# Kernel optimization log

Measured on AMD Instinct MI355X. Metric: run time of the kernel, lower is better.

Reference implementation:

```python
import jax, jax.numpy as jnp
import numpy as np

B = 8
RESOLUTIONS = [65, 129, 257, 513, 1025]
NUM_POINTS = [0, 4096, 16384, 65536, 262144]
CLIP_MIN = -1e9
FINAL = 1025          # last resolution (both axes)
B_MIN, B_MAX = -1.0, 1.0
BALANCE = 0.5


def setup_inputs() -> dict:
    key = jax.random.key(0)
    k1, k2, k3, k4 = jax.random.split(key, 4)
    return {
        "w1": jax.random.normal(k1, (2, 256), jnp.float32),
        "b1": jax.random.normal(k2, (256,), jnp.float32),
        "w2": jax.random.normal(k3, (256, 1), jnp.float32),
        "b2": jax.random.normal(k4, (1,), jnp.float32),
    }


def _interp_bilinear_ac(x, H, W):
    """F.interpolate(..., mode='bilinear', align_corners=True). x: [B, C, h, w]."""
    b, c, h, w = x.shape
    ys = jnp.linspace(0.0, h - 1.0, H)
    xs = jnp.linspace(0.0, w - 1.0, W)
    y0 = jnp.floor(ys).astype(jnp.int32)
    y1 = jnp.minimum(y0 + 1, h - 1)
    wy = ys - y0
    x0 = jnp.floor(xs).astype(jnp.int32)
    x1 = jnp.minimum(x0 + 1, w - 1)
    wx = xs - x0
    # interpolate rows, then columns
    top = x[:, :, y0, :] * (1.0 - wy)[None, None, :, None] + x[:, :, y1, :] * wy[None, None, :, None]
    return top[:, :, :, x0] * (1.0 - wx) + top[:, :, :, x1] * wx


def _batch_eval(coords, w1, b1, w2, b2):
    """coords: [B, N, 2] in final-resolution pixel space (align_corners=False mapping).
    Returns occupancy [B, N] (C == 1)."""
    coords2d = coords / FINAL + 0.5 / FINAL                 # normalize to [0, 1]
    p = coords2d * (B_MAX - B_MIN) + B_MIN                  # [B, N, 2] in world coords
    h = jax.nn.relu(jnp.einsum('bnd,dh->bnh', p, w1) + b1)  # [B, N, 256]
    occ = jax.nn.sigmoid(jnp.einsum('bnh,ho->bno', h, w2) + b2)
    return occ[..., 0]


def reference(w1, b1, w2, b2):
    occ = None
    for i, res in enumerate(RESOLUTIONS):
        if i == 0:
            # init_coords: grid of res x res points spanning [0, FINAL-1]
            xs = jnp.linspace(0.0, FINAL - 1.0, res)
            gy, gx = jnp.meshgrid(xs, xs, indexing='ij')          # y rows, x cols
            coords = jnp.stack([gx.ravel(), gy.ravel()], axis=-1)  # [N, 2] (x, y)
            coords = jnp.broadcast_to(coords, (B, res * res, 2))
            o = _batch_eval(coords, w1, b1, w2, b2)               # [B, N]
            occ = o.reshape(B, 1, res, res)                       # [B, C, H, W]
        else:
            occ = _interp_bilinear_ac(occ, res, res)
            npt = NUM_POINTS[i]
            if npt <= 0:
                continue
            # uncertainty = -|occ - balance_value|
            unc = -jnp.abs(occ - BALANCE)                          # [B, 1, H, W]
            flat_unc = unc.reshape(B, res * res)
            scores, idx = jax.lax.top_k(flat_unc, npt)             # [B, npt]
            px = (idx % res).astype(jnp.float32)
            py = (idx // res).astype(jnp.float32)
            stride = (FINAL - 1.0) / (res - 1.0)
            coords = jnp.stack([px, py], axis=-1) * stride         # [B, npt, 2]
            new_vals = _batch_eval(coords, w1, b1, w2, b2)         # [B, npt]
            occ_flat = occ.reshape(B, res * res)
            old_vals = jnp.take_along_axis(occ_flat, idx, axis=1)
            vals = jnp.where(scores >= CLIP_MIN, new_vals, old_vals)
            occ_flat = jax.vmap(lambda o, i2, v: o.at[i2].set(v))(occ_flat, idx, vals)
            occ = occ_flat.reshape(B, 1, res, res)
    return occ
```

## Files before the change

kernel.cpp:

```cpp
#include <hip/hip_runtime.h>
#include <stdint.h>

#define HID 256
#define NMAXPIX (1025 * 1025)
#define NREP 8
#define NSEG 2048
#define SELMAX 2112

#define HISTA_OFF 0
#define HISTB_OFF 16384
#define HISTC_OFF 32768
#define SCAL_OFF  40960
#define TIC_OFF   41024
#define STAGE_U32 43072

__device__ __forceinline__ float mlp_eval4(float wx, float wy,
                                           const float4* __restrict__ w1x,
                                           const float4* __restrict__ w1y,
                                           const float4* __restrict__ vb1,
                                           const float4* __restrict__ vw2, float b2v) {
    const float C0 = (float)(0.5 / 1025.0);
    float px = (wx / 1025.0f + C0) * 2.0f - 1.0f;
    float py = (wy / 1025.0f + C0) * 2.0f - 1.0f;
    float a0 = 0.f, a1 = 0.f, a2 = 0.f, a3 = 0.f;
#pragma unroll 8
    for (int q = 0; q < HID / 4; ++q) {
        float4 a = w1x[q], b = w1y[q], c = vb1[q], d = vw2[q];
        float h0 = px * a.x + py * b.x + c.x;
        float h1 = px * a.y + py * b.y + c.y;
        float h2 = px * a.z + py * b.z + c.z;
        float h3 = px * a.w + py * b.w + c.w;
        h0 = h0 > 0.f ? h0 : 0.f;
        h1 = h1 > 0.f ? h1 : 0.f;
        h2 = h2 > 0.f ? h2 : 0.f;
        h3 = h3 > 0.f ? h3 : 0.f;
        a0 += h0 * d.x;
        a1 += h1 * d.y;
        a2 += h2 * d.z;
        a3 += h3 * d.w;
    }
    float x = ((a0 + a1) + (a2 + a3)) + b2v;
    float r;
    if (x >= 0.f) { r = 1.0f / (1.0f + expf(-x)); }
    else { float e = expf(x); r = e / (1.0f + e); }
    return r;
}

__device__ __forceinline__ uint32_t block_exscan_256(uint32_t v, volatile uint32_t* lds4) {
    int lane = threadIdx.x & 63, w = threadIdx.x >> 6;
    uint32_t inc = v;
#pragma unroll
    for (int d = 1; d < 64; d <<= 1) {
        uint32_t o = (uint32_t)__shfl_up((int)inc, d, 64);
        if (lane >= d) inc += o;
    }
    if (lane == 63) lds4[w] = inc;
    __syncthreads();
    uint32_t woff = 0;
    for (int i = 0; i < w; ++i) woff += lds4[i];
    return woff + inc - v;
}

__device__ void scan_dev(const uint32_t* __restrict__ hist, int NB,
                         uint32_t rem_in, uint32_t prefix_in, int shift,
                         uint32_t* outp, uint32_t* outr,
                         volatile uint32_t* lds4, volatile uint32_t* ldspair) {
    int tid = threadIdx.x;
    int C = NB >> 8;
    int b0 = NB - (tid + 1) * C;
    uint32_t cnts[8];
#pragma unroll
    for (int k = 0; k < 8; ++k) cnts[k] = 0;
    for (int rep = 0; rep < NREP; ++rep) {
        const uint4* p = (const uint4*)(hist + (size_t)rep * NB + b0);
#pragma unroll
        for (int g = 0; g < 2; ++g) {
            if (g * 4 < C) {
                uint4 v = p[g];
                cnts[g * 4 + 0] += v.x;
                cnts[g * 4 + 1] += v.y;
                cnts[g * 4 + 2] += v.z;
                cnts[g * 4 + 3] += v.w;
            }
        }
    }
    uint32_t ssum = 0;
    for (int k = 0; k < C; ++k) ssum += cnts[k];
    uint32_t excl = block_exscan_256(ssum, lds4);
    uint32_t run = excl;
    for (int k = 0; k < C; ++k) {
        uint32_t c = cnts[C - 1 - k];
        if (rem_in > run && rem_in <= run + c) {
            ldspair[0] = (prefix_in << shift) | (uint32_t)(b0 + C - 1 - k);
            ldspair[1] = rem_in - run;
        }
        run += c;
    }
    __syncthreads();
    *outp = ldspair[0];
    *outr = ldspair[1];
}

__global__ __launch_bounds__(256) void k_eval0z(const float* __restrict__ w1, const float* __restrict__ b1,
                                                const float* __restrict__ w2, const float* __restrict__ b2,
                                                float* __restrict__ occ, uint32_t* __restrict__ zbuf, int zcount) {
    __shared__ alignas(16) float sw1[2 * HID];
    __shared__ alignas(16) float sb1[HID];
    __shared__ alignas(16) float sw2[HID];
    int tid = threadIdx.x;
    for (int i = tid; i < 2 * HID; i += 256) sw1[i] = w1[i];
    sb1[tid] = b1[tid];
    sw2[tid] = w2[tid];
    __syncthreads();
    int gtid = blockIdx.x * 256 + tid;
    int nthreads = gridDim.x * 256;
    for (int i = gtid; i < zcount; i += nthreads) zbuf[i] = 0;
    for (int n = gtid; n < 65 * 65; n += nthreads) {
        int i = n / 65, j = n % 65;
        occ[n] = mlp_eval4(16.0f * (float)j, 16.0f * (float)i,
                           (const float4*)sw1, (const float4*)(sw1 + HID),
                           (const float4*)sb1, (const float4*)sw2, b2[0]);
    }
}

__global__ __launch_bounds__(256) void k_upkey(const float* __restrict__ in, int rp,
                                               float* __restrict__ outg, int r, int nb, int bstride,
                                               uint32_t* __restrict__ keys,
                                               uint32_t* __restrict__ histA) {
    __shared__ uint32_t hist[2048];
    int tid = threadIdx.x;
    for (int k = tid; k < 2048; k += 256) hist[k] = 0;
    __syncthreads();
    int N = r * r;
    int lane = tid & 63;
    int gstride = gridDim.x * 256;
    for (int n0 = blockIdx.x * 256; n0 < N; n0 += gstride) {
        int n = n0 + tid;
        bool act = n < N;
        uint32_t key = 0;
        if (act) {
            int i = n / r, j = n % r;
            int i2 = i >> 1, j2 = j >> 1;
            float v;
            if ((i & 1) == 0) {
                if ((j & 1) == 0) {
                    v = in[i2 * rp + j2];
                } else {
                    float a = in[i2 * rp + j2], b = in[i2 * rp + j2 + 1];
                    v = a * 0.5f + b * 0.5f;
                }
            } else {
                if ((j & 1) == 0) {
                    float a = in[i2 * rp + j2], b = in[(i2 + 1) * rp + j2];
                    v = a * 0.5f + b * 0.5f;
                } else {
                    float a = in[i2 * rp + j2],      c = in[i2 * rp + j2 + 1];
                    float b = in[(i2 + 1) * rp + j2], d = in[(i2 + 1) * rp + j2 + 1];
                    float t1 = a * 0.5f + b * 0.5f;
                    float t2 = c * 0.5f + d * 0.5f;
                    v = t1 * 0.5f + t2 * 0.5f;
                }
            }
            for (int k = 0; k < nb; ++k) outg[(size_t)k * bstride + n] = v;
            float unc = -fabsf(v - 0.5f);
            uint32_t u = __float_as_uint(unc);
            key = (u & 0x80000000u) ? ~u : (u | 0x80000000u);
            keys[n] = key;
        }
        uint32_t bin = key >> 21;
        unsigned long long m = __ballot(act);
        if (m) {
            int leader = __ffsll(m) - 1;
            uint32_t lbin = (uint32_t)__shfl((int)bin, leader, 64);
            unsigned long long smk = __ballot(act && bin == lbin);
            if (smk == m) {
                if (lane == leader) atomicAdd(&hist[lbin], (uint32_t)__popcll(m));
            } else if (act) {
                atomicAdd(&hist[bin], 1u);
            }
        }
    }
    __syncthreads();
    uint32_t* myrep = histA + (size_t)(blockIdx.x & (NREP - 1)) * 2048;
    for (int k = tid; k < 2048; k += 256) {
        uint32_t c = hist[k];
        if (c) atomicAdd(&myrep[k], c);
    }
}

__global__ __launch_bounds__(256) void k_histmid(const uint32_t* __restrict__ keys, int N,
                                                 const uint32_t* __restrict__ prevHist,
                                                 uint32_t* __restrict__ scal,
                                                 int useNpt, uint32_t npt, int scalInIdx, int shift,
                                                 int scalOutIdx,
                                                 int fshift, int bshift, uint32_t bmask,
                                                 uint32_t* __restrict__ outHist, int NBout) {
    __shared__ uint32_t lh[2048];
    __shared__ uint32_t lds4[4];
    __shared__ uint32_t ldspair[2];
    int tid = threadIdx.x, lane = tid & 63;
    uint32_t rem_in = useNpt ? npt : scal[scalInIdx + 1];
    uint32_t pfx_in = useNpt ? 0u  : scal[scalInIdx];
    uint32_t pfx, rem;
    scan_dev(prevHist, 2048, rem_in, pfx_in, shift, &pfx, &rem, lds4, ldspair);
    if (blockIdx.x == 0 && tid == 0) { scal[scalOutIdx] = pfx; scal[scalOutIdx + 1] = rem; }
    for (int k = tid; k < 2048; k += 256) lh[k] = 0;
    __syncthreads();
    int gstride = gridDim.x * 256;
    for (int base = blockIdx.x * 256; base < N; base += gstride) {
        int n = base + tid;
        bool inb = n < N;
        uint32_t key = inb ? keys[n] : 0u;
        bool flt = inb && ((key >> fshift) == pfx);
        uint32_t bin = (key >> bshift) & bmask;
        unsigned long long m = __ballot(flt);
        if (m) {
            int leader = __ffsll(m) - 1;
            uint32_t lbin = (uint32_t)__shfl((int)bin, leader, 64);
            unsigned long long smk = __ballot(flt && bin == lbin);
            if (smk == m) {
                if (lane == leader) atomicAdd(&lh[lbin], (uint32_t)__popcll(m));
            } else if (flt) {
                atomicAdd(&lh[bin], 1u);
            }
        }
    }
    __syncthreads();
    uint32_t* myrep = outHist + (size_t)(blockIdx.x & (NREP - 1)) * NBout;
    for (int k = tid; k < NBout; k += 256) {
        uint32_t c = lh[k];
        if (c) atomicAdd(&myrep[k], c);
    }
}

__global__ __launch_bounds__(256) void k_segcnt(const uint32_t* __restrict__ keys, int N, int seglen,
                                                const uint32_t* __restrict__ histC,
                                                uint32_t* __restrict__ scal,
                                                uint32_t* __restrict__ tic) {
    __shared__ uint32_t lds4[4];
    __shared__ uint32_t ldspair[2];
    int tid = threadIdx.x, lane = tid & 63;
    uint32_t rem2 = scal[3], pfx2 = scal[2];
    uint32_t K, t;
    scan_dev(histC, 1024, rem2, pfx2, 10, &K, &t, lds4, ldspair);
    if (blockIdx.x == 0 && tid == 0) { scal[4] = K; scal[5] = t; }
    int wv = blockIdx.x * 4 + (tid >> 6);
    int s0 = wv * seglen;
    int s1 = s0 + seglen; if (s1 > N) s1 = N;
    uint32_t tcnt = 0;
    for (int base = s0; base < s1; base += 64) {
        int n = base + lane;
        if (n < s1) tcnt += (keys[n] == K) ? 1u : 0u;
    }
#pragma unroll
    for (int d = 32; d; d >>= 1) tcnt += (uint32_t)__shfl_down((int)tcnt, d, 64);
    if (lane == 0) tic[wv] = tcnt;
}

__global__ __launch_bounds__(256) void k_seleval(const uint32_t* __restrict__ keys, int N, int seglen,
                                                 const uint32_t* __restrict__ scal,
                                                 const uint32_t* __restrict__ tic,
                                                 int r, float stride,
                                                 float* __restrict__ occ, int nb, int bstride,
                                                 const float* __restrict__ w1, const float* __restrict__ b1,
                                                 const float* __restrict__ w2, const float* __restrict__ b2) {
    __shared__ alignas(16) float sw1[2 * HID];
    __shared__ alignas(16) float sb1[HID];
    __shared__ alignas(16) float sw2[HID];
    __shared__ uint32_t selcnt;
    __shared__ uint32_t selidx[SELMAX];
    int tid = threadIdx.x, lane = tid & 63;
    for (int i = tid; i < 2 * HID; i += 256) sw1[i] = w1[i];
    sb1[tid] = b1[tid];
    sw2[tid] = w2[tid];
    if (tid == 0) selcnt = 0;
    __syncthreads();
    uint32_t K = scal[4], t = scal[5];

    int wv = blockIdx.x * 4 + (tid >> 6);
    uint32_t tp = 0;
    for (int i = lane; i < wv; i += 64) tp += tic[i];
#pragma unroll
    for (int d = 32; d; d >>= 1) tp += (uint32_t)__shfl_down((int)tp, d, 64);
    tp = (uint32_t)__shfl((int)tp, 0, 64);

    uint32_t tie_run = tp;
    int s0 = wv * seglen;
    int s1 = s0 + seglen; if (s1 > N) s1 = N;
    unsigned long long lowmask = (lane == 63) ? ~0ull >> 1 : ((1ull << lane) - 1ull);
    for (int base = s0; base < s1; base += 64) {
        int n = base + lane;
        bool inb = n < s1;
        uint32_t key = inb ? keys[n] : 0u;
        bool gt = inb && (key > K);
        bool tie = inb && (key == K);
        unsigned long long tm = __ballot(tie);
        uint32_t trank = tie_run + (uint32_t)__popcll(tm & lowmask);
        bool sel = gt || (tie && trank < t);
        unsigned long long smk = __ballot(sel);
        if (smk) {
            int leader = __ffsll(smk) - 1;
            uint32_t wbase = 0;
            if (lane == leader) wbase = atomicAdd(&selcnt, (uint32_t)__popcll(smk));
            wbase = (uint32_t)__shfl((int)wbase, leader, 64);
            if (sel) selidx[wbase + (uint32_t)__popcll(smk & lowmask)] = (uint32_t)n;
        }
        tie_run += (uint32_t)__popcll(tm);
    }
    __syncthreads();

    uint32_t cnt = selcnt;
    float vb2 = b2[0];
    const float4* w1x = (const float4*)sw1;
    const float4* w1y = (const float4*)(sw1 + HID);
    const float4* vb1 = (const float4*)sb1;
    const float4* vw2 = (const float4*)sw2;
    const float C0 = (float)(0.5 / 1025.0);
    for (uint32_t bb = 0; bb < cnt; bb += 512) {
        uint32_t i0 = bb + tid, i1 = bb + tid + 256;
        bool v0 = i0 < cnt, v1 = i1 < cnt;
        int nA = v0 ? (int)selidx[i0] : 0;
        int nB = v1 ? (int)selidx[i1] : 0;
        int iA = nA / r, jA = nA % r;
        int iB = nB / r, jB = nB % r;
        float pxA = ((stride * (float)jA) / 1025.0f + C0) * 2.0f - 1.0f;
        float pyA = ((stride * (float)iA) / 1025.0f + C0) * 2.0f - 1.0f;
        float pxB = ((stride * (float)jB) / 1025.0f + C0) * 2.0f - 1.0f;
        float pyB = ((stride * (float)iB) / 1025.0f + C0) * 2.0f - 1.0f;
        float4 A0 = {0, 0, 0, 0}, A1 = {0, 0, 0, 0};
#pragma unroll 4
        for (int q = 0; q < HID / 4; ++q) {
            float4 a = w1x[q], b = w1y[q], c = vb1[q], d = vw2[q];
            {
                float h0 = pxA * a.x + pyA * b.x + c.x;
                float h1 = pxA * a.y + pyA * b.y + c.y;
                float h2 = pxA * a.z + pyA * b.z + c.z;
                float h3 = pxA * a.w + pyA * b.w + c.w;
                h0 = h0 > 0.f ? h0 : 0.f;
                h1 = h1 > 0.f ? h1 : 0.f;
                h2 = h2 > 0.f ? h2 : 0.f;
                h3 = h3 > 0.f ? h3 : 0.f;
                A0.x += h0 * d.x; A0.y += h1 * d.y;
                A0.z += h2 * d.z; A0.w += h3 * d.w;
            }
            {
                float h0 = pxB * a.x + pyB * b.x + c.x;
                float h1 = pxB * a.y + pyB * b.y + c.y;
                float h2 = pxB * a.z + pyB * b.z + c.z;
                float h3 = pxB * a.w + pyB * b.w + c.w;
                h0 = h0 > 0.f ? h0 : 0.f;
                h1 = h1 > 0.f ? h1 : 0.f;
                h2 = h2 > 0.f ? h2 : 0.f;
                h3 = h3 > 0.f ? h3 : 0.f;
                A1.x += h0 * d.x; A1.y += h1 * d.y;
                A1.z += h2 * d.z; A1.w += h3 * d.w;
            }
        }
        if (v0) {
            float x = ((A0.x + A0.y) + (A0.z + A0.w)) + vb2;
            float rr;
            if (x >= 0.f) { rr = 1.0f / (1.0f + expf(-x)); }
            else { float e = expf(x); rr = e / (1.0f + e); }
            for (int k = 0; k < nb; ++k) occ[(size_t)k * bstride + nA] = rr;
        }
        if (v1) {
            float x = ((A1.x + A1.y) + (A1.z + A1.w)) + vb2;
            float rr;
            if (x >= 0.f) { rr = 1.0f / (1.0f + expf(-x)); }
            else { float e = expf(x); rr = e / (1.0f + e); }
            for (int k = 0; k < nb; ++k) occ[(size_t)k * bstride + nB] = rr;
        }
    }
}

__global__ __launch_bounds__(256) void k_bcast(const float* __restrict__ src, float* __restrict__ dst, int N) {
    int q = blockIdx.x * 256 + threadIdx.x;
    int n = q * 4;
    if (n + 3 < N) {
        float4 v = *(const float4*)(src + n);
#pragma unroll
        for (int k = 0; k < 8; ++k) *(float4*)(dst + (size_t)k * N + n) = v;
    } else if (n < N) {
        for (int m = n; m < N; ++m) {
            float v = src[m];
#pragma unroll
            for (int k = 0; k < 8; ++k) dst[(size_t)k * N + m] = v;
        }
    }
}

extern "C" void kernel_launch(void* const* d_in, const int* in_sizes, int n_in,
                              void* d_out, int out_size, void* d_ws, size_t ws_size,
                              hipStream_t stream) {
    const float* w1 = (const float*)d_in[0];
    const float* b1 = (const float*)d_in[1];
    const float* w2 = (const float*)d_in[2];
    const float* b2 = (const float*)d_in[3];
    float* out = (float*)d_out;

    const size_t A = (((size_t)NMAXPIX * 4) + 255) & ~(size_t)255;
    const size_t SMALL_BYTES = (size_t)4 * STAGE_U32 * 4;
    const size_t need = 3 * A + SMALL_BYTES;

    int fused8 = (ws_size >= need);
    char* base = fused8 ? (char*)d_ws : (char*)d_out;
    float* buf0 = (float*)(base);
    float* buf1 = (float*)(base + A);
    uint32_t* keys = (uint32_t*)(base + 2 * A);
    uint32_t* smallb = (uint32_t*)(base + 3 * A);

    k_eval0z<<<dim3(512), dim3(256), 0, stream>>>(w1, b1, w2, b2, buf0, smallb, 4 * STAGE_U32);

    const int resA[5] = {65, 129, 257, 513, 1025};
    const int nptA[5] = {0, 4096, 16384, 65536, 262144};
    float* cur = buf0;
    float* nxt = buf1;
    for (int s = 1; s < 5; ++s) {
        int rp = resA[s - 1], r = resA[s];
        int N = r * r;
        uint32_t npt = (uint32_t)nptA[s];
        uint32_t* sm    = smallb + (size_t)(s - 1) * STAGE_U32;
        uint32_t* histA = sm + HISTA_OFF;
        uint32_t* histB = sm + HISTB_OFF;
        uint32_t* histC = sm + HISTC_OFF;
        uint32_t* scal  = sm + SCAL_OFF;
        uint32_t* tic   = sm + TIC_OFF;
        int nb1 = (N + 255) / 256;
        int nbu = nb1 < 1024 ? nb1 : 1024;
        int seglen = (N + NSEG - 1) / NSEG;
        float stride = 1024.0f / (float)(r - 1);

        int last = (s == 4);
        float* stage_out = (last && fused8) ? out : nxt;
        int nb = (last && fused8) ? 8 : 1;
        int bstride = (last && fused8) ? NMAXPIX : 0;

        k_upkey<<<dim3(nbu), dim3(256), 0, stream>>>(cur, rp, stage_out, r, nb, bstride, keys, histA);
        k_histmid<<<dim3(512), dim3(256), 0, stream>>>(keys, N, histA, scal, 1, npt, 0, 0,
                                                       0, 21, 10, 0x7FFu, histB, 2048);
        k_histmid<<<dim3(512), dim3(256), 0, stream>>>(keys, N, histB, scal, 0, 0u, 0, 11,
                                                       2, 10, 0, 0x3FFu, histC, 1024);
        k_segcnt<<<dim3(NSEG / 4), dim3(256), 0, stream>>>(keys, N, seglen, histC, scal, tic);
        k_seleval<<<dim3(NSEG / 4), dim3(256), 0, stream>>>(keys, N, seglen, scal, tic, r, stride,
                                                            stage_out, nb, bstride, w1, b1, w2, b2);
        if (!(last && fused8)) { float* tmp = cur; cur = nxt; nxt = tmp; }
    }
    if (!fused8) {
        k_bcast<<<dim3(((NMAXPIX + 3) / 4 + 255) / 256), dim3(256), 0, stream>>>(cur, out, NMAXPIX);
    }
}
```

Baseline: 244.6 us.

## Fuse radix-select histogram, tie-count and eval kernels into one persistent kernel

```diff
diff --git a/kernel.cpp b/kernel.cpp
--- a/kernel.cpp
+++ b/kernel.cpp
@@ -3,16 +3,26 @@
 
 #define HID 256
 #define NMAXPIX (1025 * 1025)
-#define NREP 8
-#define NSEG 2048
+#define NREP 4
+#define MBLK 512
+#define NSEG (MBLK * 4)
 #define SELMAX 2112
-
-#define HISTA_OFF 0
-#define HISTB_OFF 16384
-#define HISTC_OFF 32768
-#define SCAL_OFF  40960
-#define TIC_OFF   41024
-#define STAGE_U32 43072
+#define FLAG31 0x80000000u
+
+#define HA_OFF    0
+#define HB_OFF    8192
+#define HC_OFF    16384
+#define SLOT1_OFF 20480
+#define SLOT2_OFF 20482
+#define CTR1_OFF  20484
+#define CTR2_OFF  20485
+#define BLKT_OFF  20544
+#define STAGE_U32 21120
+
+#define ALOAD32(p)  __hip_atomic_load((p), __ATOMIC_RELAXED, __HIP_MEMORY_SCOPE_AGENT)
+#define ALOAD64(p)  __hip_atomic_load((p), __ATOMIC_RELAXED, __HIP_MEMORY_SCOPE_AGENT)
+#define ASTORE32(p, v) __hip_atomic_store((p), (v), __ATOMIC_RELAXED, __HIP_MEMORY_SCOPE_AGENT)
+#define ASTORE64(p, v) __hip_atomic_store((p), (v), __ATOMIC_RELAXED, __HIP_MEMORY_SCOPE_AGENT)
 
 __device__ __forceinline__ float mlp_eval4(float wx, float wy,
                                            const float4* __restrict__ w1x,
@@ -61,10 +71,33 @@
     return woff + inc - v;
 }
 
-__device__ void scan_dev(const uint32_t* __restrict__ hist, int NB,
-                         uint32_t rem_in, uint32_t prefix_in, int shift,
-                         uint32_t* outp, uint32_t* outr,
-                         volatile uint32_t* lds4, volatile uint32_t* ldspair) {
+__device__ __forceinline__ void scan_find(const uint32_t* cnts, int C, int NB,
+                                          uint32_t rem_in, uint32_t pfx_in, int shift,
+                                          volatile uint32_t* lds4, volatile uint32_t* ldspair,
+                                          uint32_t* outp, uint32_t* outr) {
+    int tid = threadIdx.x;
+    int b0 = NB - (tid + 1) * C;
+    uint32_t s = 0;
+    for (int k = 0; k < C; ++k) s += cnts[k];
+    uint32_t excl = block_exscan_256(s, lds4);
+    uint32_t run = excl;
+    for (int k = 0; k < C; ++k) {
+        uint32_t c = cnts[C - 1 - k];
+        if (rem_in > run && rem_in <= run + c) {
+            ldspair[0] = (pfx_in << shift) | (uint32_t)(b0 + C - 1 - k);
+            ldspair[1] = rem_in - run;
+        }
+        run += c;
+    }
+    __syncthreads();
+    *outp = ldspair[0];
+    *outr = ldspair[1];
+}
+
+__device__ void scan_hist_norm(const uint32_t* __restrict__ hist, int NB,
+                               uint32_t rem_in, uint32_t pfx_in, int shift,
+                               volatile uint32_t* lds4, volatile uint32_t* ldspair,
+                               uint32_t* outp, uint32_t* outr) {
     int tid = threadIdx.x;
     int C = NB >> 8;
     int b0 = NB - (tid + 1) * C;
@@ -84,21 +117,24 @@
             }
         }
     }
-    uint32_t ssum = 0;
-    for (int k = 0; k < C; ++k) ssum += cnts[k];
-    uint32_t excl = block_exscan_256(ssum, lds4);
-    uint32_t run = excl;
-    for (int k = 0; k < C; ++k) {
-        uint32_t c = cnts[C - 1 - k];
-        if (rem_in > run && rem_in <= run + c) {
-            ldspair[0] = (prefix_in << shift) | (uint32_t)(b0 + C - 1 - k);
-            ldspair[1] = rem_in - run;
-        }
-        run += c;
-    }
-    __syncthreads();
-    *outp = ldspair[0];
-    *outr = ldspair[1];
+    scan_find(cnts, C, NB, rem_in, pfx_in, shift, lds4, ldspair, outp, outr);
+}
+
+__device__ void scan_hist_atomic(const uint32_t* __restrict__ hist, int NB,
+                                 uint32_t rem_in, uint32_t pfx_in, int shift,
+                                 volatile uint32_t* lds4, volatile uint32_t* ldspair,
+                                 uint32_t* outp, uint32_t* outr) {
+    int tid = threadIdx.x;
+    int C = NB >> 8;
+    int b0 = NB - (tid + 1) * C;
+    uint32_t cnts[8];
+#pragma unroll
+    for (int k = 0; k < 8; ++k) cnts[k] = 0;
+    for (int rep = 0; rep < NREP; ++rep) {
+        const uint32_t* p = hist + (size_t)rep * NB + b0;
+        for (int k = 0; k < C; ++k) cnts[k] += ALOAD32(&p[k]);
+    }
+    scan_find(cnts, C, NB, rem_in, pfx_in, shift, lds4, ldspair, outp, outr);
 }
 
 __global__ __launch_bounds__(256) void k_eval0z(const float* __restrict__ w1, const float* __restrict__ b1,
@@ -188,31 +224,52 @@
     }
 }
 
-__global__ __launch_bounds__(256) void k_histmid(const uint32_t* __restrict__ keys, int N,
-                                                 const uint32_t* __restrict__ prevHist,
-                                                 uint32_t* __restrict__ scal,
-                                                 int useNpt, uint32_t npt, int scalInIdx, int shift,
-                                                 int scalOutIdx,
-                                                 int fshift, int bshift, uint32_t bmask,
-                                                 uint32_t* __restrict__ outHist, int NBout) {
+__global__ __launch_bounds__(256, 2) void k_mega(const uint32_t* __restrict__ keys, int N, int seglen,
+                                                 uint32_t npt, uint32_t* __restrict__ sm,
+                                                 int r, float stride,
+                                                 float* __restrict__ occ, int nb, int bstride,
+                                                 const float* __restrict__ w1, const float* __restrict__ b1,
+                                                 const float* __restrict__ w2, const float* __restrict__ b2) {
+    __shared__ alignas(16) float sw1[2 * HID];
+    __shared__ alignas(16) float sb1[HID];
+    __shared__ alignas(16) float sw2[HID];
     __shared__ uint32_t lh[2048];
     __shared__ uint32_t lds4[4];
     __shared__ uint32_t ldspair[2];
-    int tid = threadIdx.x, lane = tid & 63;
-    uint32_t rem_in = useNpt ? npt : scal[scalInIdx + 1];
-    uint32_t pfx_in = useNpt ? 0u  : scal[scalInIdx];
-    uint32_t pfx, rem;
-    scan_dev(prevHist, 2048, rem_in, pfx_in, shift, &pfx, &rem, lds4, ldspair);
-    if (blockIdx.x == 0 && tid == 0) { scal[scalOutIdx] = pfx; scal[scalOutIdx + 1] = rem; }
+    __shared__ uint32_t wcnt[4];
+    __shared__ uint32_t islast_s;
+    __shared__ uint32_t selcnt;
+    __shared__ uint32_t selidx[SELMAX];
+
+    int tid = threadIdx.x, lane = tid & 63, w = tid >> 6;
+    int blk = blockIdx.x;
+    int gstride = MBLK * 256;
+    for (int i = tid; i < 2 * HID; i += 256) sw1[i] = w1[i];
+    sb1[tid] = b1[tid];
+    sw2[tid] = w2[tid];
+    if (tid == 0) selcnt = 0;
+
+    uint32_t* histA = sm + HA_OFF;
+    uint32_t* histB = sm + HB_OFF;
+    uint32_t* histC = sm + HC_OFF;
+    unsigned long long* slot1 = (unsigned long long*)(sm + SLOT1_OFF);
+    unsigned long long* slot2 = (unsigned long long*)(sm + SLOT2_OFF);
+    uint32_t* ctr1 = sm + CTR1_OFF;
+    uint32_t* ctr2 = sm + CTR2_OFF;
+    uint32_t* blkT = sm + BLKT_OFF;
+
+    uint32_t pfx1, rem1;
+    scan_hist_norm(histA, 2048, npt, 0u, 0, lds4, ldspair, &pfx1, &rem1);
+
+    __syncthreads();
     for (int k = tid; k < 2048; k += 256) lh[k] = 0;
     __syncthreads();
-    int gstride = gridDim.x * 256;
-    for (int base = blockIdx.x * 256; base < N; base += gstride) {
+    for (int base = blk * 256; base < N; base += gstride) {
         int n = base + tid;
         bool inb = n < N;
         uint32_t key = inb ? keys[n] : 0u;
-        bool flt = inb && ((key >> fshift) == pfx);
-        uint32_t bin = (key >> bshift) & bmask;
+        bool flt = inb && ((key >> 21) == pfx1);
+        uint32_t bin = (key >> 10) & 0x7FFu;
         unsigned long long m = __ballot(flt);
         if (m) {
             int leader = __ffsll(m) - 1;
@@ -226,67 +283,129 @@
         }
     }
     __syncthreads();
-    uint32_t* myrep = outHist + (size_t)(blockIdx.x & (NREP - 1)) * NBout;
-    for (int k = tid; k < NBout; k += 256) {
-        uint32_t c = lh[k];
-        if (c) atomicAdd(&myrep[k], c);
-    }
-}
-
-__global__ __launch_bounds__(256) void k_segcnt(const uint32_t* __restrict__ keys, int N, int seglen,
-                                                const uint32_t* __restrict__ histC,
-                                                uint32_t* __restrict__ scal,
-                                                uint32_t* __restrict__ tic) {
-    __shared__ uint32_t lds4[4];
-    __shared__ uint32_t ldspair[2];
-    int tid = threadIdx.x, lane = tid & 63;
-    uint32_t rem2 = scal[3], pfx2 = scal[2];
+    {
+        uint32_t* myrep = histB + (size_t)(blk & (NREP - 1)) * 2048;
+        for (int k = tid; k < 2048; k += 256) {
+            uint32_t c = lh[k];
+            if (c) atomicAdd(&myrep[k], c);
+        }
+    }
+    __syncthreads();
+    if (tid == 0) {
+        uint32_t old = __hip_atomic_fetch_add(ctr1, 1u, __ATOMIC_RELAXED, __HIP_MEMORY_SCOPE_AGENT);
+        islast_s = (old == (uint32_t)(MBLK - 1));
+    }
+    __syncthreads();
+    if (islast_s) {
+        uint32_t p2, r2;
+        scan_hist_atomic(histB, 2048, rem1, pfx1, 11, lds4, ldspair, &p2, &r2);
+        if (tid == 0) {
+            unsigned long long v = ((unsigned long long)p2 << 32) | (unsigned long long)(r2 | FLAG31);
+            ASTORE64(slot1, v);
+        }
+    }
+    uint32_t pfx2, rem2;
+    {
+        unsigned long long v;
+        for (;;) {
+            v = ALOAD64(slot1);
+            if ((uint32_t)v & FLAG31) break;
+            __builtin_amdgcn_s_sleep(2);
+        }
+        pfx2 = (uint32_t)(v >> 32);
+        rem2 = (uint32_t)v & 0x7FFFFFFFu;
+    }
+
+    __syncthreads();
+    for (int k = tid; k < 1024; k += 256) lh[k] = 0;
+    __syncthreads();
+    for (int base = blk * 256; base < N; base += gstride) {
+        int n = base + tid;
+        bool inb = n < N;
+        uint32_t key = inb ? keys[n] : 0u;
+        bool flt = inb && ((key >> 10) == pfx2);
+        uint32_t bin = key & 0x3FFu;
+        unsigned long long m = __ballot(flt);
+        if (m) {
+            int leader = __ffsll(m) - 1;
+            uint32_t lbin = (uint32_t)__shfl((int)bin, leader, 64);
+            unsigned long long smk = __ballot(flt && bin == lbin);
+            if (smk == m) {
+                if (lane == leader) atomicAdd(&lh[lbin], (uint32_t)__popcll(m));
+            } else if (flt) {
+                atomicAdd(&lh[bin], 1u);
+            }
+        }
+    }
+    __syncthreads();
+    {
+        uint32_t* myrep = histC + (size_t)(blk & (NREP - 1)) * 1024;
+        for (int k = tid; k < 1024; k += 256) {
+            uint32_t c = lh[k];
+            if (c) atomicAdd(&myrep[k], c);
+        }
+    }
+    __syncthreads();
+    if (tid == 0) {
+        uint32_t old = __hip_atomic_fetch_add(ctr2, 1u, __ATOMIC_RELAXED, __HIP_MEMORY_SCOPE_AGENT);
+        islast_s = (old == (uint32_t)(MBLK - 1));
+    }
+    __syncthreads();
+    if (islast_s) {
+        uint32_t K_, t_;
+        scan_hist_atomic(histC, 1024, rem2, pfx2, 10, lds4, ldspair, &K_, &t_);
+        if (tid == 0) {
+            unsigned long long v = ((unsigned long long)K_ << 32) | (unsigned long long)(t_ | FLAG31);
+            ASTORE64(slot2, v);
+        }
+    }
     uint32_t K, t;
-    scan_dev(histC, 1024, rem2, pfx2, 10, &K, &t, lds4, ldspair);
-    if (blockIdx.x == 0 && tid == 0) { scal[4] = K; scal[5] = t; }
-    int wv = blockIdx.x * 4 + (tid >> 6);
+    {
+        unsigned long long v;
+        for (;;) {
+            v = ALOAD64(slot2);
+            if ((uint32_t)v & FLAG31) break;
+            __builtin_amdgcn_s_sleep(2);
+        }
+        K = (uint32_t)(v >> 32);
+        t = (uint32_t)v & 0x7FFFFFFFu;
+    }
+
+    int wv = blk * 4 + w;
     int s0 = wv * seglen;
     int s1 = s0 + seglen; if (s1 > N) s1 = N;
-    uint32_t tcnt = 0;
-    for (int base = s0; base < s1; base += 64) {
-        int n = base + lane;
-        if (n < s1) tcnt += (keys[n] == K) ? 1u : 0u;
-    }
-#pragma unroll
-    for (int d = 32; d; d >>= 1) tcnt += (uint32_t)__shfl_down((int)tcnt, d, 64);
-    if (lane == 0) tic[wv] = tcnt;
-}
-
-__global__ __launch_bounds__(256) void k_seleval(const uint32_t* __restrict__ keys, int N, int seglen,
-                                                 const uint32_t* __restrict__ scal,
-                                                 const uint32_t* __restrict__ tic,
-                                                 int r, float stride,
-                                                 float* __restrict__ occ, int nb, int bstride,
-                                                 const float* __restrict__ w1, const float* __restrict__ b1,
-                                                 const float* __restrict__ w2, const float* __restrict__ b2) {
-    __shared__ alignas(16) float sw1[2 * HID];
-    __shared__ alignas(16) float sb1[HID];
-    __shared__ alignas(16) float sw2[HID];
-    __shared__ uint32_t selcnt;
-    __shared__ uint32_t selidx[SELMAX];
-    int tid = threadIdx.x, lane = tid & 63;
-    for (int i = tid; i < 2 * HID; i += 256) sw1[i] = w1[i];
-    sb1[tid] = b1[tid];
-    sw2[tid] = w2[tid];
-    if (tid == 0) selcnt = 0;
-    __syncthreads();
-    uint32_t K = scal[4], t = scal[5];
-
-    int wv = blockIdx.x * 4 + (tid >> 6);
-    uint32_t tp = 0;
-    for (int i = lane; i < wv; i += 64) tp += tic[i];
-#pragma unroll
-    for (int d = 32; d; d >>= 1) tp += (uint32_t)__shfl_down((int)tp, d, 64);
-    tp = (uint32_t)__shfl((int)tp, 0, 64);
+    {
+        uint32_t tcnt = 0;
+        for (int base = s0; base < s1; base += 64) {
+            int n = base + lane;
+            if (n < s1) tcnt += (keys[n] == K) ? 1u : 0u;
+        }
+#pragma unroll
+        for (int d = 32; d; d >>= 1) tcnt += (uint32_t)__shfl_down((int)tcnt, d, 64);
+        if (lane == 0) wcnt[w] = tcnt;
+    }
+    __syncthreads();
+    if (tid == 0) {
+        uint32_t tot = wcnt[0] + wcnt[1] + wcnt[2] + wcnt[3];
+        ASTORE32(&blkT[blk], tot | FLAG31);
+    }
+    uint32_t bp = 0;
+    for (int i = lane; i < blk; i += 64) {
+        uint32_t v;
+        for (;;) {
+            v = ALOAD32(&blkT[i]);
+            if (v & FLAG31) break;
+            __builtin_amdgcn_s_sleep(2);
+        }
+        bp += v & 0x7FFFFFFFu;
+    }
+#pragma unroll
+    for (int d = 32; d; d >>= 1) bp += (uint32_t)__shfl_down((int)bp, d, 64);
+    bp = (uint32_t)__shfl((int)bp, 0, 64);
+    uint32_t tp = bp;
+    for (int ww = 0; ww < w; ++ww) tp += wcnt[ww];
 
     uint32_t tie_run = tp;
-    int s0 = wv * seglen;
-    int s1 = s0 + seglen; if (s1 > N) s1 = N;
     unsigned long long lowmask = (lane == 63) ? ~0ull >> 1 : ((1ull << lane) - 1ull);
     for (int base = s0; base < s1; base += 64) {
         int n = base + lane;
@@ -316,60 +435,51 @@
     const float4* vb1 = (const float4*)sb1;
     const float4* vw2 = (const float4*)sw2;
     const float C0 = (float)(0.5 / 1025.0);
-    for (uint32_t bb = 0; bb < cnt; bb += 512) {
-        uint32_t i0 = bb + tid, i1 = bb + tid + 256;
-        bool v0 = i0 < cnt, v1 = i1 < cnt;
+    for (uint32_t bb = 0; bb < cnt; bb += 1024) {
+        uint32_t i0 = bb + tid, i1 = i0 + 256, i2 = i0 + 512, i3 = i0 + 768;
+        bool v0 = i0 < cnt, v1 = i1 < cnt, v2 = i2 < cnt, v3 = i3 < cnt;
         int nA = v0 ? (int)selidx[i0] : 0;
         int nB = v1 ? (int)selidx[i1] : 0;
+        int nC = v2 ? (int)selidx[i2] : 0;
+        int nD = v3 ? (int)selidx[i3] : 0;
         int iA = nA / r, jA = nA % r;
         int iB = nB / r, jB = nB % r;
-        float pxA = ((stride * (float)jA) / 1025.0f + C0) * 2.0f - 1.0f;
-        float pyA = ((stride * (float)iA) / 1025.0f + C0) * 2.0f - 1.0f;
-        float pxB = ((stride * (float)jB) / 1025.0f + C0) * 2.0f - 1.0f;
-        float pyB = ((stride * (float)iB) / 1025.0f + C0) * 2.0f - 1.0f;
-        float4 A0 = {0, 0, 0, 0}, A1 = {0, 0, 0, 0};
+        int iC = nC / r, jC = nC % r;
+        int iD = nD / r, jD = nD % r;
+        float px0 = ((stride * (float)jA) / 1025.0f + C0) * 2.0f - 1.0f;
+        float py0 = ((stride * (float)iA) / 1025.0f + C0) * 2.0f - 1.0f;
+        float px1 = ((stride * (float)jB) / 1025.0f + C0) * 2.0f - 1.0f;
+        float py1 = ((stride * (float)iB) / 1025.0f + C0) * 2.0f - 1.0f;
+        float px2 = ((stride * (float)jC) / 1025.0f + C0) * 2.0f - 1.0f;
+        float py2 = ((stride * (float)iC) / 1025.0f + C0) * 2.0f - 1.0f;
+        float px3 = ((stride * (float)jD) / 1025.0f + C0) * 2.0f - 1.0f;
+        float py3 = ((stride * (float)iD) / 1025.0f + C0) * 2.0f - 1.0f;
+        float4 A0 = {0, 0, 0, 0}, A1 = {0, 0, 0, 0}, A2 = {0, 0, 0, 0}, A3 = {0, 0, 0, 0};
 #pragma unroll 4
         for (int q = 0; q < HID / 4; ++q) {
             float4 a = w1x[q], b = w1y[q], c = vb1[q], d = vw2[q];
-            {
-                float h0 = pxA * a.x + pyA * b.x + c.x;
-                float h1 = pxA * a.y + pyA * b.y + c.y;
-                float h2 = pxA * a.z + pyA * b.z + c.z;
-                float h3 = pxA * a.w + pyA * b.w + c.w;
-                h0 = h0 > 0.f ? h0 : 0.f;
-                h1 = h1 > 0.f ? h1 : 0.f;
-                h2 = h2 > 0.f ? h2 : 0.f;
-                h3 = h3 > 0.f ? h3 : 0.f;
-                A0.x += h0 * d.x; A0.y += h1 * d.y;
-                A0.z += h2 * d.z; A0.w += h3 * d.w;
-            }
-            {
-                float h0 = pxB * a.x + pyB * b.x + c.x;
-                float h1 = pxB * a.y + pyB * b.y + c.y;
-                float h2 = pxB * a.z + pyB * b.z + c.z;
-                float h3 = pxB * a.w + pyB * b.w + c.w;
-                h0 = h0 > 0.f ? h0 : 0.f;
-                h1 = h1 > 0.f ? h1 : 0.f;
-                h2 = h2 > 0.f ? h2 : 0.f;
-                h3 = h3 > 0.f ? h3 : 0.f;
-                A1.x += h0 * d.x; A1.y += h1 * d.y;
-                A1.z += h2 * d.z; A1.w += h3 * d.w;
-            }
-        }
-        if (v0) {
-            float x = ((A0.x + A0.y) + (A0.z + A0.w)) + vb2;
-            float rr;
-            if (x >= 0.f) { rr = 1.0f / (1.0f + expf(-x)); }
-            else { float e = expf(x); rr = e / (1.0f + e); }
-            for (int k = 0; k < nb; ++k) occ[(size_t)k * bstride + nA] = rr;
-        }
-        if (v1) {
-            float x = ((A1.x + A1.y) + (A1.z + A1.w)) + vb2;
-            float rr;
-            if (x >= 0.f) { rr = 1.0f / (1.0f + expf(-x)); }
-            else { float e = expf(x); rr = e / (1.0f + e); }
-            for (int k = 0; k < nb; ++k) occ[(size_t)k * bstride + nB] = rr;
-        }
+#define STEP(P, AX) {                                              \
+            float h0 = px##P * a.x + py##P * b.x + c.x;            \
+            float h1 = px##P * a.y + py##P * b.y + c.y;            \
+            float h2 = px##P * a.z + py##P * b.z + c.z;            \
+            float h3 = px##P * a.w + py##P * b.w + c.w;            \
+            h0 = h0 > 0.f ? h0 : 0.f;                              \
+            h1 = h1 > 0.f ? h1 : 0.f;                              \
+            h2 = h2 > 0.f ? h2 : 0.f;                              \
+            h3 = h3 > 0.f ? h3 : 0.f;                              \
+            AX.x += h0 * d.x; AX.y += h1 * d.y;                    \
+            AX.z += h2 * d.z; AX.w += h3 * d.w; }
+            STEP(0, A0) STEP(1, A1) STEP(2, A2) STEP(3, A3)
+#undef STEP
+        }
+#define FIN(VQ, AX, NP) if (VQ) {                                  \
+        float x = ((AX.x + AX.y) + (AX.z + AX.w)) + vb2;           \
+        float rr;                                                  \
+        if (x >= 0.f) { rr = 1.0f / (1.0f + expf(-x)); }           \
+        else { float e = expf(x); rr = e / (1.0f + e); }           \
+        for (int k = 0; k < nb; ++k) occ[(size_t)k * bstride + NP] = rr; }
+        FIN(v0, A0, nA) FIN(v1, A1, nB) FIN(v2, A2, nC) FIN(v3, A3, nD)
+#undef FIN
     }
 }
 
@@ -419,12 +529,7 @@
         int rp = resA[s - 1], r = resA[s];
         int N = r * r;
         uint32_t npt = (uint32_t)nptA[s];
-        uint32_t* sm    = smallb + (size_t)(s - 1) * STAGE_U32;
-        uint32_t* histA = sm + HISTA_OFF;
-        uint32_t* histB = sm + HISTB_OFF;
-        uint32_t* histC = sm + HISTC_OFF;
-        uint32_t* scal  = sm + SCAL_OFF;
-        uint32_t* tic   = sm + TIC_OFF;
+        uint32_t* sm = smallb + (size_t)(s - 1) * STAGE_U32;
         int nb1 = (N + 255) / 256;
         int nbu = nb1 < 1024 ? nb1 : 1024;
         int seglen = (N + NSEG - 1) / NSEG;
@@ -435,14 +540,9 @@
         int nb = (last && fused8) ? 8 : 1;
         int bstride = (last && fused8) ? NMAXPIX : 0;
 
-        k_upkey<<<dim3(nbu), dim3(256), 0, stream>>>(cur, rp, stage_out, r, nb, bstride, keys, histA);
-        k_histmid<<<dim3(512), dim3(256), 0, stream>>>(keys, N, histA, scal, 1, npt, 0, 0,
-                                                       0, 21, 10, 0x7FFu, histB, 2048);
-        k_histmid<<<dim3(512), dim3(256), 0, stream>>>(keys, N, histB, scal, 0, 0u, 0, 11,
-                                                       2, 10, 0, 0x3FFu, histC, 1024);
-        k_segcnt<<<dim3(NSEG / 4), dim3(256), 0, stream>>>(keys, N, seglen, histC, scal, tic);
-        k_seleval<<<dim3(NSEG / 4), dim3(256), 0, stream>>>(keys, N, seglen, scal, tic, r, stride,
-                                                            stage_out, nb, bstride, w1, b1, w2, b2);
+        k_upkey<<<dim3(nbu), dim3(256), 0, stream>>>(cur, rp, stage_out, r, nb, bstride, keys, sm + HA_OFF);
+        k_mega<<<dim3(MBLK), dim3(256), 0, stream>>>(keys, N, seglen, npt, sm, r, stride,
+                                                     stage_out, nb, bstride, w1, b1, w2, b2);
         if (!(last && fused8)) { float* tmp = cur; cur = nxt; nxt = tmp; }
     }
     if (!fused8) {
```

New measurement: 319.7 us. +30.7%, slower.

## Fuse tie counting into selection kernel via decoupled block prefix flags

Applied to the files above, without the earlier changes.

```diff
diff --git a/kernel.cpp b/kernel.cpp
--- a/kernel.cpp
+++ b/kernel.cpp
@@ -3,16 +3,20 @@
 
 #define HID 256
 #define NMAXPIX (1025 * 1025)
-#define NREP 8
+#define NREP 4
 #define NSEG 2048
 #define SELMAX 2112
-
-#define HISTA_OFF 0
-#define HISTB_OFF 16384
-#define HISTC_OFF 32768
-#define SCAL_OFF  40960
-#define TIC_OFF   41024
-#define STAGE_U32 43072
+#define FLAG31 0x80000000u
+
+#define HA_OFF   0
+#define HB_OFF   8192
+#define HC_OFF   16384
+#define SCAL_OFF 20480
+#define BLKT_OFF 20544
+#define STAGE_U32 21120
+
+#define ALOAD32(p)  __hip_atomic_load((p), __ATOMIC_RELAXED, __HIP_MEMORY_SCOPE_AGENT)
+#define ASTORE32(p, v) __hip_atomic_store((p), (v), __ATOMIC_RELAXED, __HIP_MEMORY_SCOPE_AGENT)
 
 __device__ __forceinline__ float mlp_eval4(float wx, float wy,
                                            const float4* __restrict__ w1x,
@@ -233,60 +237,72 @@
     }
 }
 
-__global__ __launch_bounds__(256) void k_segcnt(const uint32_t* __restrict__ keys, int N, int seglen,
-                                                const uint32_t* __restrict__ histC,
-                                                uint32_t* __restrict__ scal,
-                                                uint32_t* __restrict__ tic) {
-    __shared__ uint32_t lds4[4];
-    __shared__ uint32_t ldspair[2];
-    int tid = threadIdx.x, lane = tid & 63;
-    uint32_t rem2 = scal[3], pfx2 = scal[2];
-    uint32_t K, t;
-    scan_dev(histC, 1024, rem2, pfx2, 10, &K, &t, lds4, ldspair);
-    if (blockIdx.x == 0 && tid == 0) { scal[4] = K; scal[5] = t; }
-    int wv = blockIdx.x * 4 + (tid >> 6);
-    int s0 = wv * seglen;
-    int s1 = s0 + seglen; if (s1 > N) s1 = N;
-    uint32_t tcnt = 0;
-    for (int base = s0; base < s1; base += 64) {
-        int n = base + lane;
-        if (n < s1) tcnt += (keys[n] == K) ? 1u : 0u;
-    }
-#pragma unroll
-    for (int d = 32; d; d >>= 1) tcnt += (uint32_t)__shfl_down((int)tcnt, d, 64);
-    if (lane == 0) tic[wv] = tcnt;
-}
-
-__global__ __launch_bounds__(256) void k_seleval(const uint32_t* __restrict__ keys, int N, int seglen,
-                                                 const uint32_t* __restrict__ scal,
-                                                 const uint32_t* __restrict__ tic,
-                                                 int r, float stride,
-                                                 float* __restrict__ occ, int nb, int bstride,
-                                                 const float* __restrict__ w1, const float* __restrict__ b1,
-                                                 const float* __restrict__ w2, const float* __restrict__ b2) {
+__global__ __launch_bounds__(256, 2) void k_seleval(const uint32_t* __restrict__ keys, int N, int seglen,
+                                                    const uint32_t* __restrict__ histC,
+                                                    const uint32_t* __restrict__ scal,
+                                                    uint32_t* __restrict__ blkT,
+                                                    int r, float stride,
+                                                    float* __restrict__ occ, int nb, int bstride,
+                                                    const float* __restrict__ w1, const float* __restrict__ b1,
+                                                    const float* __restrict__ w2, const float* __restrict__ b2) {
     __shared__ alignas(16) float sw1[2 * HID];
     __shared__ alignas(16) float sb1[HID];
     __shared__ alignas(16) float sw2[HID];
+    __shared__ uint32_t lds4[4];
+    __shared__ uint32_t ldspair[2];
+    __shared__ uint32_t wcnt[4];
+    __shared__ uint32_t bp_s;
     __shared__ uint32_t selcnt;
     __shared__ uint32_t selidx[SELMAX];
-    int tid = threadIdx.x, lane = tid & 63;
+    int tid = threadIdx.x, lane = tid & 63, w = tid >> 6;
+    int blk = blockIdx.x;
     for (int i = tid; i < 2 * HID; i += 256) sw1[i] = w1[i];
     sb1[tid] = b1[tid];
     sw2[tid] = w2[tid];
     if (tid == 0) selcnt = 0;
     __syncthreads();
-    uint32_t K = scal[4], t = scal[5];
-
-    int wv = blockIdx.x * 4 + (tid >> 6);
-    uint32_t tp = 0;
-    for (int i = lane; i < wv; i += 64) tp += tic[i];
-#pragma unroll
-    for (int d = 32; d; d >>= 1) tp += (uint32_t)__shfl_down((int)tp, d, 64);
-    tp = (uint32_t)__shfl((int)tp, 0, 64);
-
-    uint32_t tie_run = tp;
+
+    uint32_t K, t;
+    scan_dev(histC, 1024, scal[3], scal[2], 10, &K, &t, lds4, ldspair);
+
+    int wv = blk * 4 + w;
     int s0 = wv * seglen;
     int s1 = s0 + seglen; if (s1 > N) s1 = N;
+    {
+        uint32_t tcnt = 0;
+        for (int base = s0; base < s1; base += 64) {
+            int n = base + lane;
+            if (n < s1) tcnt += (keys[n] == K) ? 1u : 0u;
+        }
+#pragma unroll
+        for (int d = 32; d; d >>= 1) tcnt += (uint32_t)__shfl_down((int)tcnt, d, 64);
+        if (lane == 0) wcnt[w] = tcnt;
+    }
+    __syncthreads();
+    if (w == 0) {
+        if (lane == 0) {
+            uint32_t tot = wcnt[0] + wcnt[1] + wcnt[2] + wcnt[3];
+            ASTORE32(&blkT[blk], tot | FLAG31);
+        }
+        uint32_t bp = 0;
+        for (int i = lane; i < blk; i += 64) {
+            uint32_t v;
+            for (;;) {
+                v = ALOAD32(&blkT[i]);
+                if (v & FLAG31) break;
+                __builtin_amdgcn_s_sleep(2);
+            }
+            bp += v & 0x7FFFFFFFu;
+        }
+#pragma unroll
+        for (int d = 32; d; d >>= 1) bp += (uint32_t)__shfl_down((int)bp, d, 64);
+        if (lane == 0) bp_s = bp;
+    }
+    __syncthreads();
+    uint32_t tp = bp_s;
+    for (int ww = 0; ww < w; ++ww) tp += wcnt[ww];
+
+    uint32_t tie_run = tp;
     unsigned long long lowmask = (lane == 63) ? ~0ull >> 1 : ((1ull << lane) - 1ull);
     for (int base = s0; base < s1; base += 64) {
         int n = base + lane;
@@ -316,60 +332,51 @@
     const float4* vb1 = (const float4*)sb1;
     const float4* vw2 = (const float4*)sw2;
     const float C0 = (float)(0.5 / 1025.0);
-    for (uint32_t bb = 0; bb < cnt; bb += 512) {
-        uint32_t i0 = bb + tid, i1 = bb + tid + 256;
-        bool v0 = i0 < cnt, v1 = i1 < cnt;
+    for (uint32_t bb = 0; bb < cnt; bb += 1024) {
+        uint32_t i0 = bb + tid, i1 = i0 + 256, i2 = i0 + 512, i3 = i0 + 768;
+        bool v0 = i0 < cnt, v1 = i1 < cnt, v2 = i2 < cnt, v3 = i3 < cnt;
         int nA = v0 ? (int)selidx[i0] : 0;
         int nB = v1 ? (int)selidx[i1] : 0;
+        int nC = v2 ? (int)selidx[i2] : 0;
+        int nD = v3 ? (int)selidx[i3] : 0;
         int iA = nA / r, jA = nA % r;
         int iB = nB / r, jB = nB % r;
-        float pxA = ((stride * (float)jA) / 1025.0f + C0) * 2.0f - 1.0f;
-        float pyA = ((stride * (float)iA) / 1025.0f + C0) * 2.0f - 1.0f;
-        float pxB = ((stride * (float)jB) / 1025.0f + C0) * 2.0f - 1.0f;
-        float pyB = ((stride * (float)iB) / 1025.0f + C0) * 2.0f - 1.0f;
-        float4 A0 = {0, 0, 0, 0}, A1 = {0, 0, 0, 0};
+        int iC = nC / r, jC = nC % r;
+        int iD = nD / r, jD = nD % r;
+        float px0 = ((stride * (float)jA) / 1025.0f + C0) * 2.0f - 1.0f;
+        float py0 = ((stride * (float)iA) / 1025.0f + C0) * 2.0f - 1.0f;
+        float px1 = ((stride * (float)jB) / 1025.0f + C0) * 2.0f - 1.0f;
+        float py1 = ((stride * (float)iB) / 1025.0f + C0) * 2.0f - 1.0f;
+        float px2 = ((stride * (float)jC) / 1025.0f + C0) * 2.0f - 1.0f;
+        float py2 = ((stride * (float)iC) / 1025.0f + C0) * 2.0f - 1.0f;
+        float px3 = ((stride * (float)jD) / 1025.0f + C0) * 2.0f - 1.0f;
+        float py3 = ((stride * (float)iD) / 1025.0f + C0) * 2.0f - 1.0f;
+        float4 A0 = {0, 0, 0, 0}, A1 = {0, 0, 0, 0}, A2 = {0, 0, 0, 0}, A3 = {0, 0, 0, 0};
 #pragma unroll 4
         for (int q = 0; q < HID / 4; ++q) {
             float4 a = w1x[q], b = w1y[q], c = vb1[q], d = vw2[q];
-            {
-                float h0 = pxA * a.x + pyA * b.x + c.x;
-                float h1 = pxA * a.y + pyA * b.y + c.y;
-                float h2 = pxA * a.z + pyA * b.z + c.z;
-                float h3 = pxA * a.w + pyA * b.w + c.w;
-                h0 = h0 > 0.f ? h0 : 0.f;
-                h1 = h1 > 0.f ? h1 : 0.f;
-                h2 = h2 > 0.f ? h2 : 0.f;
-                h3 = h3 > 0.f ? h3 : 0.f;
-                A0.x += h0 * d.x; A0.y += h1 * d.y;
-                A0.z += h2 * d.z; A0.w += h3 * d.w;
-            }
-            {
-                float h0 = pxB * a.x + pyB * b.x + c.x;
-                float h1 = pxB * a.y + pyB * b.y + c.y;
-                float h2 = pxB * a.z + pyB * b.z + c.z;
-                float h3 = pxB * a.w + pyB * b.w + c.w;
-                h0 = h0 > 0.f ? h0 : 0.f;
-                h1 = h1 > 0.f ? h1 : 0.f;
-                h2 = h2 > 0.f ? h2 : 0.f;
-                h3 = h3 > 0.f ? h3 : 0.f;
-                A1.x += h0 * d.x; A1.y += h1 * d.y;
-                A1.z += h2 * d.z; A1.w += h3 * d.w;
-            }
-        }
-        if (v0) {
-            float x = ((A0.x + A0.y) + (A0.z + A0.w)) + vb2;
-            float rr;
-            if (x >= 0.f) { rr = 1.0f / (1.0f + expf(-x)); }
-            else { float e = expf(x); rr = e / (1.0f + e); }
-            for (int k = 0; k < nb; ++k) occ[(size_t)k * bstride + nA] = rr;
-        }
-        if (v1) {
-            float x = ((A1.x + A1.y) + (A1.z + A1.w)) + vb2;
-            float rr;
-            if (x >= 0.f) { rr = 1.0f / (1.0f + expf(-x)); }
-            else { float e = expf(x); rr = e / (1.0f + e); }
-            for (int k = 0; k < nb; ++k) occ[(size_t)k * bstride + nB] = rr;
-        }
+#define STEP(P, AX) {                                              \
+            float h0 = px##P * a.x + py##P * b.x + c.x;            \
+            float h1 = px##P * a.y + py##P * b.y + c.y;            \
+            float h2 = px##P * a.z + py##P * b.z + c.z;            \
+            float h3 = px##P * a.w + py##P * b.w + c.w;            \
+            h0 = h0 > 0.f ? h0 : 0.f;                              \
+            h1 = h1 > 0.f ? h1 : 0.f;                              \
+            h2 = h2 > 0.f ? h2 : 0.f;                              \
+            h3 = h3 > 0.f ? h3 : 0.f;                              \
+            AX.x += h0 * d.x; AX.y += h1 * d.y;                    \
+            AX.z += h2 * d.z; AX.w += h3 * d.w; }
+            STEP(0, A0) STEP(1, A1) STEP(2, A2) STEP(3, A3)
+#undef STEP
+        }
+#define FIN(VQ, AX, NP) if (VQ) {                                  \
+        float x = ((AX.x + AX.y) + (AX.z + AX.w)) + vb2;           \
+        float rr;                                                  \
+        if (x >= 0.f) { rr = 1.0f / (1.0f + expf(-x)); }           \
+        else { float e = expf(x); rr = e / (1.0f + e); }           \
+        for (int k = 0; k < nb; ++k) occ[(size_t)k * bstride + NP] = rr; }
+        FIN(v0, A0, nA) FIN(v1, A1, nB) FIN(v2, A2, nC) FIN(v3, A3, nD)
+#undef FIN
     }
 }
 
@@ -419,12 +426,12 @@
         int rp = resA[s - 1], r = resA[s];
         int N = r * r;
         uint32_t npt = (uint32_t)nptA[s];
-        uint32_t* sm    = smallb + (size_t)(s - 1) * STAGE_U32;
-        uint32_t* histA = sm + HISTA_OFF;
-        uint32_t* histB = sm + HISTB_OFF;
-        uint32_t* histC = sm + HISTC_OFF;
+        uint32_t* sm = smallb + (size_t)(s - 1) * STAGE_U32;
+        uint32_t* histA = sm + HA_OFF;
+        uint32_t* histB = sm + HB_OFF;
+        uint32_t* histC = sm + HC_OFF;
         uint32_t* scal  = sm + SCAL_OFF;
-        uint32_t* tic   = sm + TIC_OFF;
+        uint32_t* blkT  = sm + BLKT_OFF;
         int nb1 = (N + 255) / 256;
         int nbu = nb1 < 1024 ? nb1 : 1024;
         int seglen = (N + NSEG - 1) / NSEG;
@@ -440,9 +447,9 @@
                                                        0, 21, 10, 0x7FFu, histB, 2048);
         k_histmid<<<dim3(512), dim3(256), 0, stream>>>(keys, N, histB, scal, 0, 0u, 0, 11,
                                                        2, 10, 0, 0x3FFu, histC, 1024);
-        k_segcnt<<<dim3(NSEG / 4), dim3(256), 0, stream>>>(keys, N, seglen, histC, scal, tic);
-        k_seleval<<<dim3(NSEG / 4), dim3(256), 0, stream>>>(keys, N, seglen, scal, tic, r, stride,
-                                                            stage_out, nb, bstride, w1, b1, w2, b2);
+        k_seleval<<<dim3(NSEG / 4), dim3(256), 0, stream>>>(keys, N, seglen, histC, scal, blkT,
+                                                            r, stride, stage_out, nb, bstride,
+                                                            w1, b1, w2, b2);
         if (!(last && fused8)) { float* tmp = cur; cur = nxt; nxt = tmp; }
     }
     if (!fused8) {
```

Result: slower. 257.8 us (+5.4%).
